# Kernel optimization log

Measured on AMD Instinct MI355X. Metric: run time of the kernel, lower is better.

Reference implementation:

```python
import jax, jax.numpy as jnp
import numpy as np

B, N, C = 4, 8192, 512
H, Dh, G, R = 8, 64, 64, 2  # heads, dim_head, slice_num, mlp_ratio
EPS_LN = 1e-5
EPS_NORM = 1e-5


def _ln(x, g, b):
    m = jnp.mean(x, axis=-1, keepdims=True)
    v = jnp.var(x, axis=-1, keepdims=True)
    return (x - m) * jax.lax.rsqrt(v + EPS_LN) * g + b


def setup_inputs() -> dict:
    key = jax.random.key(0)
    ks = jax.random.split(key, 16)
    r = lambda k, shp: jax.random.normal(k, shp, jnp.float32) * 0.02
    inner = H * Dh
    return {
        "fx": jax.random.normal(ks[0], (B, N, C), jnp.float32),
        "ln1_g": jnp.ones((C,), jnp.float32), "ln1_b": jnp.zeros((C,), jnp.float32),
        "Wx": r(ks[1], (C, inner)), "bx": jnp.zeros((inner,), jnp.float32),
        "Wfx": r(ks[2], (C, inner)), "bfx": jnp.zeros((inner,), jnp.float32),
        "Wslice": r(ks[3], (Dh, G)), "bslice": jnp.zeros((G,), jnp.float32),
        "temperature": jnp.full((1, H, 1, 1), 0.5, jnp.float32),
        "Wq": r(ks[4], (Dh, Dh)), "Wk": r(ks[5], (Dh, Dh)), "Wv": r(ks[6], (Dh, Dh)),
        "Wout": r(ks[7], (inner, C)), "bout": jnp.zeros((C,), jnp.float32),
        "tln_g": jnp.ones((Dh,), jnp.float32), "tln_b": jnp.zeros((Dh,), jnp.float32),
        "Wm1": r(ks[8], (Dh, R * Dh)), "bm1": jnp.zeros((R * Dh,), jnp.float32),
        "Wm2": r(ks[9], (R * Dh, Dh)), "bm2": jnp.zeros((Dh,), jnp.float32),
    }


def reference(fx, ln1_g, ln1_b, Wx, bx, Wfx, bfx, Wslice, bslice, temperature,
              Wq, Wk, Wv, Wout, bout, tln_g, tln_b, Wm1, bm1, Wm2, bm2):
    fx_norm = _ln(fx, ln1_g, ln1_b)                          # [B,N,C]
    # _forward_slice: project to per-head mid features
    x_mid = (fx_norm @ Wx + bx).reshape(B, N, H, Dh).transpose(0, 2, 1, 3)   # [B,H,N,Dh]
    fx_mid = (fx_norm @ Wfx + bfx).reshape(B, N, H, Dh).transpose(0, 2, 1, 3)
    # _project_token: soft slice assignment + weighted pooling into G tokens
    logits = jnp.einsum('bhnd,dg->bhng', x_mid, Wslice) + bslice
    slice_w = jax.nn.softmax(logits / temperature, axis=-1)  # [B,H,N,G]
    slice_norm = jnp.sum(slice_w, axis=2)                    # [B,H,G]
    slice_tok = jnp.einsum('bhnd,bhng->bhgd', fx_mid, slice_w) / (slice_norm[..., None] + EPS_NORM)
    # attention over the small token set (G tokens)
    q = slice_tok @ Wq
    k = slice_tok @ Wk
    v = slice_tok @ Wv
    scale = Dh ** -0.5
    attn = jax.nn.softmax(jnp.einsum('bhgd,bhpd->bhgp', q, k) * scale, axis=-1)
    out_tok = jnp.einsum('bhgp,bhpd->bhgd', attn, v) + slice_tok
    # token MLP with residual
    h = _ln(out_tok, tln_g, tln_b)
    h = jax.nn.gelu(h @ Wm1 + bm1, approximate=False) @ Wm2 + bm2
    tokens = h + out_tok                                     # [B,H,G,Dh]
    # _deslice: weighted scatter back to N points, merge heads, out projection
    out_x = jnp.einsum('bhgd,bhng->bhnd', tokens, slice_w)
    out_x = out_x.transpose(0, 2, 1, 3).reshape(B, N, H * Dh)
    out = out_x @ Wout + bout
    return out + fx_norm
```

## Files before the change

### kernel.cpp

```cpp
#include <hip/hip_runtime.h>
#include <math.h>

#define B_ 4
#define N_ 8192
#define C_ 512
#define H_ 8
#define M_ (B_ * N_)

typedef __attribute__((ext_vector_type(8))) short bf16x8;
typedef __attribute__((ext_vector_type(4))) float f32x4;
typedef __attribute__((ext_vector_type(8))) unsigned short u16x8;
typedef __attribute__((ext_vector_type(4))) unsigned short u16x4;

__device__ __forceinline__ float b2f(unsigned short u) {
  union { unsigned int i; float f; } v;
  v.i = ((unsigned int)u) << 16;
  return v.f;
}
__device__ __forceinline__ unsigned short f2b(float f) {
  union { float f; unsigned int i; } v;
  v.f = f;
  unsigned int r = v.i + 0x7fff + ((v.i >> 16) & 1);
  return (unsigned short)(r >> 16);
}
__device__ __forceinline__ void gl_lds16(const void* g, void* l) {
  __builtin_amdgcn_global_load_lds(
      (const __attribute__((address_space(1))) unsigned int*)g,
      (__attribute__((address_space(3))) unsigned int*)l, 16, 0, 0);
}

__global__ __launch_bounds__(256) void ln_bf16(
    const float* __restrict__ x, const float* __restrict__ gam,
    const float* __restrict__ bet, unsigned short* __restrict__ y) {
  int wave = threadIdx.x >> 6, lane = threadIdx.x & 63;
  int row = (blockIdx.x << 2) + wave;
  const float4* xr = (const float4*)(x + (size_t)row * C_);
  float4 v0 = xr[lane], v1 = xr[lane + 64];
  float s = v0.x + v0.y + v0.z + v0.w + v1.x + v1.y + v1.z + v1.w;
  float q = v0.x * v0.x + v0.y * v0.y + v0.z * v0.z + v0.w * v0.w +
            v1.x * v1.x + v1.y * v1.y + v1.z * v1.z + v1.w * v1.w;
#pragma unroll
  for (int off = 32; off; off >>= 1) {
    s += __shfl_xor(s, off);
    q += __shfl_xor(q, off);
  }
  float mean = s * (1.0f / C_);
  float var = q * (1.0f / C_) - mean * mean;
  float rstd = rsqrtf(var + 1e-5f);
  const float4* gr = (const float4*)gam;
  const float4* br = (const float4*)bet;
  float4 g0 = gr[lane], g1 = gr[lane + 64];
  float4 b0 = br[lane], b1 = br[lane + 64];
  u16x4 oa, ob;
  oa.x = f2b((v0.x - mean) * rstd * g0.x + b0.x);
  oa.y = f2b((v0.y - mean) * rstd * g0.y + b0.y);
  oa.z = f2b((v0.z - mean) * rstd * g0.z + b0.z);
  oa.w = f2b((v0.w - mean) * rstd * g0.w + b0.w);
  ob.x = f2b((v1.x - mean) * rstd * g1.x + b1.x);
  ob.y = f2b((v1.y - mean) * rstd * g1.y + b1.y);
  ob.z = f2b((v1.z - mean) * rstd * g1.z + b1.z);
  ob.w = f2b((v1.w - mean) * rstd * g1.w + b1.w);
  unsigned short* yr = y + (size_t)row * C_;
  *(u16x4*)(yr + (lane << 2)) = oa;
  *(u16x4*)(yr + 256 + (lane << 2)) = ob;
}

__global__ __launch_bounds__(256) void prep_all(
    const float* __restrict__ Wx, const float* __restrict__ Wfx,
    const float* __restrict__ Wout, const float* __restrict__ Wsl,
    const float* __restrict__ Wq, const float* __restrict__ Wk,
    const float* __restrict__ Wv, const float* __restrict__ Wm1,
    const float* __restrict__ Wm2, unsigned short* __restrict__ WtX,
    unsigned short* __restrict__ WtF, unsigned short* __restrict__ WtO,
    unsigned short* __restrict__ wsf, unsigned short* __restrict__ wfr) {
  __shared__ float tile[64][65];
  int blk = blockIdx.x, t = threadIdx.x;
  if (blk < 192) {
    int which = blk >> 6, sub = blk & 63;
    const float* W = (which == 0) ? Wx : (which == 1) ? Wfx : Wout;
    unsigned short* Wt = (which == 0) ? WtX : (which == 1) ? WtF : WtO;
    int r0 = (sub >> 3) << 6, c0 = (sub & 7) << 6;
    int lr = t >> 4, lc = (t & 15) << 2;
#pragma unroll
    for (int p = 0; p < 4; p++) {
      float4 v = *(const float4*)(W + (size_t)(r0 + lr + p * 16) * 512 + c0 + lc);
      tile[lr + p * 16][lc + 0] = v.x;
      tile[lr + p * 16][lc + 1] = v.y;
      tile[lr + p * 16][lc + 2] = v.z;
      tile[lr + p * 16][lc + 3] = v.w;
    }
    __syncthreads();
    int on = t >> 2, ok = (t & 3) << 4;
    unsigned short tmp[16];
#pragma unroll
    for (int j = 0; j < 16; j++) tmp[j] = f2b(tile[ok + j][on]);
    unsigned short* op = Wt + (size_t)(c0 + on) * 512 + r0 + ok;
#pragma unroll
    for (int j4 = 0; j4 < 4; j4++)
      *(u16x4*)(op + (j4 << 2)) = *(u16x4*)(tmp + (j4 << 2));
  } else {
#pragma unroll
    for (int i = 0; i < 2; i++) {
      int idx = t + i * 256;
      int f = idx >> 6, l = idx & 63;
      int gt = f >> 1, ks = f & 1;
      int g = (gt << 4) + (l & 15);
      int d0 = (ks << 5) + ((l >> 4) << 3);
      unsigned short v[8];
#pragma unroll
      for (int jj = 0; jj < 8; jj++) v[jj] = f2b(Wsl[(size_t)(d0 + jj) * 64 + g]);
      *(u16x4*)(wsf + idx * 8) = *(u16x4*)v;
      *(u16x4*)(wsf + idx * 8 + 4) = *(u16x4*)(v + 4);
    }
    for (int task = t; task < 56 * 64; task += 256) {
      int fid = task >> 6, l = task & 63;
      const float* W;
      int stride, ct, ks;
      if (fid < 24) {
        W = (fid < 8) ? Wq : (fid < 16) ? Wk : Wv;
        int e = fid & 7;
        ct = e >> 1;
        ks = e & 1;
        stride = 64;
      } else if (fid < 40) {
        W = Wm1;
        int e = fid - 24;
        ct = e >> 1;
        ks = e & 1;
        stride = 128;
      } else {
        W = Wm2;
        int e = fid - 40;
        ct = e >> 2;
        ks = e & 3;
        stride = 64;
      }
      int d0 = (ks << 5) + ((l >> 4) << 3);
      int c = (ct << 4) + (l & 15);
      unsigned short v[8];
#pragma unroll
      for (int j = 0; j < 8; j++) v[j] = f2b(W[(size_t)(d0 + j) * stride + c]);
      *(u16x4*)(wfr + task * 8) = *(u16x4*)v;
      *(u16x4*)(wfr + task * 8 + 4) = *(u16x4*)(v + 4);
    }
  }
}

template <int DEC, bool BIASROW, bool OUTBF, bool RES>
__global__ __launch_bounds__(256) void gemm_bf16(
    const unsigned short* __restrict__ A, const unsigned short* __restrict__ Bt,
    const float* __restrict__ bias, const unsigned short* __restrict__ resid,
    void* __restrict__ Cout, size_t ldC) {
  __shared__ unsigned short lds[16384];
  const int t = threadIdx.x;
  const int w = t >> 6, l = t & 63;
  int bid = blockIdx.x;
  int xcd = bid & 7, q = bid >> 3;
  int bm, bn;
  if (DEC == 0) {
    bm = ((xcd << 5) + (q >> 2)) << 7;
    bn = (q & 3) << 7;
  } else {
    bn = ((xcd << 5) + (q >> 2)) << 7;
    bm = (q & 3) << 7;
  }
  const int wm = (w >> 1) << 6, wn = (w & 1) << 6;
  f32x4 acc[4][4];
#pragma unroll
  for (int mt = 0; mt < 4; mt++)
#pragma unroll
    for (int nt = 0; nt < 4; nt++) acc[mt][nt] = (f32x4){0.f, 0.f, 0.f, 0.f};

  const int srow = t >> 3;
  const int scol = (((t & 7) ^ ((t >> 3) & 7)) << 3);
  const unsigned short* gA = A + (size_t)(bm + srow) * 512 + scol;
  const unsigned short* gB = Bt + (size_t)(bn + srow) * 512 + scol;
  const int fr = l & 15, qq = l >> 4;

  for (int k0 = 0; k0 < 512; k0 += 64) {
#pragma unroll
    for (int i = 0; i < 4; i++)
      gl_lds16(gA + (size_t)(i << 5) * 512 + k0, lds + (i << 11) + (w << 9));
#pragma unroll
    for (int i = 0; i < 4; i++)
      gl_lds16(gB + (size_t)(i << 5) * 512 + k0, lds + 8192 + (i << 11) + (w << 9));
    __syncthreads();
#pragma unroll
    for (int kk = 0; kk < 2; kk++) {
      bf16x8 af[4], bfr[4];
#pragma unroll
      for (int mt = 0; mt < 4; mt++) {
        int row = wm + mt * 16 + fr;
        af[mt] = *(const bf16x8*)&lds[row * 64 + ((((kk << 2) + qq) ^ (fr & 7)) << 3)];
      }
#pragma unroll
      for (int nt = 0; nt < 4; nt++) {
        int row = wn + nt * 16 + fr;
        bfr[nt] = *(const bf16x8*)&lds[8192 + row * 64 + ((((kk << 2) + qq) ^ (fr & 7)) << 3)];
      }
#pragma unroll
      for (int mt = 0; mt < 4; mt++)
#pragma unroll
        for (int nt = 0; nt < 4; nt++)
          acc[mt][nt] = __builtin_amdgcn_mfma_f32_16x16x32_bf16(
              af[mt], bfr[nt], acc[mt][nt], 0, 0, 0);
    }
    __syncthreads();
  }

  const int col0 = bn + wn + (l & 15);
  const int row0 = bm + wm + ((l >> 4) << 2);
#pragma unroll
  for (int mt = 0; mt < 4; mt++) {
#pragma unroll
    for (int j = 0; j < 4; j++) {
      int row = row0 + mt * 16 + j;
#pragma unroll
      for (int nt = 0; nt < 4; nt++) {
        int col = col0 + nt * 16;
        float v = acc[mt][nt][j] + (BIASROW ? bias[row] : bias[col]);
        if (RES) v += b2f(resid[(size_t)row * ldC + col]);
        if (OUTBF)
          ((unsigned short*)Cout)[(size_t)row * ldC + col] = f2b(v);
        else
          ((float*)Cout)[(size_t)row * ldC + col] = v;
      }
    }
  }
}

__global__ __launch_bounds__(256) void slice_mfma(
    unsigned short* __restrict__ xw, const unsigned short* __restrict__ wf,
    const float* __restrict__ bslice, const float* __restrict__ temp) {
  __shared__ unsigned short xs[4096];
  int t = threadIdx.x, w = t >> 6, l = t & 63;
  int blk = blockIdx.x;
  size_t base = (size_t)blk << 12;
  {
    int srow = t >> 2;
    const unsigned short* gp = xw + base + srow * 64 + ((t & 3) << 4);
    u16x8 a = *(const u16x8*)gp;
    u16x8 b = *(const u16x8*)(gp + 8);
    int sl0 = (t & 3) << 1, swz = srow & 7;
    *(u16x8*)&xs[srow * 64 + ((sl0 ^ swz) << 3)] = a;
    *(u16x8*)&xs[srow * 64 + (((sl0 + 1) ^ swz) << 3)] = b;
  }
  bf16x8 wsf[4][2];
#pragma unroll
  for (int gt = 0; gt < 4; gt++)
#pragma unroll
    for (int ks = 0; ks < 2; ks++)
      wsf[gt][ks] = *(const bf16x8*)(wf + (((gt << 1) + ks) * 64 + l) * 8);
  __syncthreads();

  int xr = (w << 4) + (l & 15);
  f32x4 acc[4];
#pragma unroll
  for (int gt = 0; gt < 4; gt++) acc[gt] = (f32x4){0.f, 0.f, 0.f, 0.f};
#pragma unroll
  for (int ks = 0; ks < 2; ks++) {
    int slot = (ks << 2) + (l >> 4);
    bf16x8 xf = *(const bf16x8*)&xs[xr * 64 + ((slot ^ (xr & 7)) << 3)];
#pragma unroll
    for (int gt = 0; gt < 4; gt++)
      acc[gt] = __builtin_amdgcn_mfma_f32_16x16x32_bf16(wsf[gt][ks], xf,
                                                        acc[gt], 0, 0, 0);
  }

  int gxr = (blk << 6) + xr;
  float invt = 1.0f / temp[gxr & 7];
  int qq = l >> 4;
  float lg[16];
  float mx = -1e30f;
#pragma unroll
  for (int gt = 0; gt < 4; gt++)
#pragma unroll
    for (int r = 0; r < 4; r++) {
      float v = (acc[gt][r] + bslice[(gt << 4) + (qq << 2) + r]) * invt;
      lg[(gt << 2) + r] = v;
      mx = fmaxf(mx, v);
    }
  mx = fmaxf(mx, __shfl_xor(mx, 16));
  mx = fmaxf(mx, __shfl_xor(mx, 32));
  float ssum = 0.f;
#pragma unroll
  for (int i = 0; i < 16; i++) {
    lg[i] = expf(lg[i] - mx);
    ssum += lg[i];
  }
  ssum += __shfl_xor(ssum, 16);
  ssum += __shfl_xor(ssum, 32);
  float inv = 1.0f / ssum;
  __syncthreads();
#pragma unroll
  for (int gt = 0; gt < 4; gt++) {
    int slot = (gt << 1) + (qq >> 1);
    int off = ((slot ^ (xr & 7)) << 3) + ((qq & 1) << 2);
    u16x4 pk;
    pk.x = f2b(lg[(gt << 2) + 0] * inv);
    pk.y = f2b(lg[(gt << 2) + 1] * inv);
    pk.z = f2b(lg[(gt << 2) + 2] * inv);
    pk.w = f2b(lg[(gt << 2) + 3] * inv);
    *(u16x4*)&xs[xr * 64 + off] = pk;
  }
  __syncthreads();
  {
    int rr = (w << 4) + (l >> 2);
    int sl = (l & 3) << 1, swz = rr & 7;
    u16x8 o0 = *(const u16x8*)&xs[rr * 64 + ((sl ^ swz) << 3)];
    u16x8 o1 = *(const u16x8*)&xs[rr * 64 + (((sl + 1) ^ swz) << 3)];
    unsigned short* op = xw + base + rr * 64 + ((l & 3) << 4);
    *(u16x8*)op = o0;
    *(u16x8*)(op + 8) = o1;
  }
}

__global__ __launch_bounds__(256) void pool_mfma(
    const unsigned short* __restrict__ sw, const unsigned short* __restrict__ fxT,
    float* __restrict__ tok_part, float* __restrict__ norm_part) {
  __shared__ unsigned short wT[4096];
  int bid = blockIdx.x;
  int bh = bid >> 4, c = bid & 15;
  int b = bh >> 3, h = bh & 7;
  int t = threadIdx.x, w = t >> 6, l = t & 63;
  int n0 = c << 9;
  const int fr15 = l & 15, fs = l >> 4;
  f32x4 acc[4];
#pragma unroll
  for (int gt = 0; gt < 4; gt++) acc[gt] = (f32x4){0.f, 0.f, 0.f, 0.f};
  float nacc[4] = {0.f, 0.f, 0.f, 0.f};

  const unsigned short* fxrow =
      fxT + (size_t)(h * 64 + w * 16 + fr15) * 32768 + b * N_ + n0 + (fs << 3);

  for (int nn = 0; nn < 512; nn += 64) {
    size_t srow = ((size_t)(b * N_ + n0 + nn + l) * 8 + h) << 6;
    u16x8 a0 = *(const u16x8*)(sw + srow + w * 16);
    u16x8 a1 = *(const u16x8*)(sw + srow + w * 16 + 8);
    __syncthreads();
#pragma unroll
    for (int j = 0; j < 16; j++) {
      int g = (w << 4) + j;
      unsigned short v = (j < 8) ? (unsigned short)a0[j] : (unsigned short)a1[j - 8];
      wT[(g << 6) + (((l >> 3) ^ (g & 7)) << 3) + (l & 7)] = v;
    }
    __syncthreads();
#pragma unroll
    for (int kk = 0; kk < 2; kk++) {
      bf16x8 bfrag = *(const bf16x8*)(fxrow + nn + (kk << 5));
#pragma unroll
      for (int gt = 0; gt < 4; gt++) {
        int g = (gt << 4) + fr15;
        int slot = (kk << 2) + fs;
        bf16x8 af = *(const bf16x8*)&wT[(g << 6) + ((slot ^ (g & 7)) << 3)];
        acc[gt] = __builtin_amdgcn_mfma_f32_16x16x32_bf16(af, bfrag, acc[gt], 0, 0, 0);
        if (w == 0) {
#pragma unroll
          for (int j = 0; j < 8; j++) nacc[gt] += b2f((unsigned short)af[j]);
        }
      }
    }
  }
  float* op = tok_part + ((size_t)bid << 12);
#pragma unroll
  for (int gt = 0; gt < 4; gt++)
#pragma unroll
    for (int rr = 0; rr < 4; rr++)
      op[((gt << 4) + (fs << 2) + rr) * 64 + (w << 4) + fr15] = acc[gt][rr];
  if (w == 0) {
#pragma unroll
    for (int gt = 0; gt < 4; gt++) {
      float s = nacc[gt];
      s += __shfl_xor(s, 16);
      s += __shfl_xor(s, 32);
      if (l < 16) norm_part[(bid << 6) + (gt << 4) + l] = s;
    }
  }
}

__global__ __launch_bounds__(256) void tok_reduce(
    const float* __restrict__ tok_part, const float* __restrict__ norm_part,
    float* __restrict__ stG) {
  int blk = blockIdx.x;
  int bh = blk >> 2, qq = blk & 3;
  int t = threadIdx.x;
  int e = (qq << 10) + (t << 2);
  int g = e >> 6;
  float s = 0.f;
  const float* np = norm_part + ((size_t)bh << 10);
#pragma unroll
  for (int c = 0; c < 16; c++) s += np[(c << 6) + g];
  float4 acc = make_float4(0.f, 0.f, 0.f, 0.f);
  const float* tp = tok_part + ((size_t)bh << 16) + e;
#pragma unroll
  for (int c = 0; c < 16; c++) {
    float4 v = *(const float4*)(tp + (c << 12));
    acc.x += v.x;
    acc.y += v.y;
    acc.z += v.z;
    acc.w += v.w;
  }
  float inv = 1.0f / (s + 1e-5f);
  acc.x *= inv;
  acc.y *= inv;
  acc.z *= inv;
  acc.w *= inv;
  *(float4*)(stG + ((size_t)bh << 12) + e) = acc;
}

__device__ __forceinline__ float gelu_exact(float x) {
  return 0.5f * x * (1.0f + erff(x * 0.70710678118654752f));
}

__global__ __launch_bounds__(256) void token_mfma(
    const float* __restrict__ stG, const unsigned short* __restrict__ wfr,
    const float* __restrict__ tg, const float* __restrict__ tb,
    const float* __restrict__ bm1, const float* __restrict__ bm2,
    unsigned short* __restrict__ wtokf) {
  __shared__ __align__(16) char smem[54272];
  unsigned short* stb = (unsigned short*)smem;
  float* st32 = (float*)(smem + 9216);
  unsigned short* hmld = (unsigned short*)(smem + 9216);
  unsigned short* qld = (unsigned short*)(smem + 26624);
  unsigned short* kld = (unsigned short*)(smem + 35840);
  unsigned short* vtl = (unsigned short*)(smem + 45056);

  int bh = blockIdx.x, t = threadIdx.x, w = t >> 6, l = t & 63;
  const int fr = l & 15, fq = l >> 4;

  {
    int r = t >> 2, c0 = (t & 3) << 4;
    const float* gp = stG + ((size_t)bh << 12) + r * 64 + c0;
    float4 a = *(const float4*)gp;
    float4 b = *(const float4*)(gp + 4);
    float4 c = *(const float4*)(gp + 8);
    float4 d = *(const float4*)(gp + 12);
    *(float4*)&st32[r * 68 + c0] = a;
    *(float4*)&st32[r * 68 + c0 + 4] = b;
    *(float4*)&st32[r * 68 + c0 + 8] = c;
    *(float4*)&st32[r * 68 + c0 + 12] = d;
    unsigned short tv[16];
    tv[0] = f2b(a.x); tv[1] = f2b(a.y); tv[2] = f2b(a.z); tv[3] = f2b(a.w);
    tv[4] = f2b(b.x); tv[5] = f2b(b.y); tv[6] = f2b(b.z); tv[7] = f2b(b.w);
    tv[8] = f2b(c.x); tv[9] = f2b(c.y); tv[10] = f2b(c.z); tv[11] = f2b(c.w);
    tv[12] = f2b(d.x); tv[13] = f2b(d.y); tv[14] = f2b(d.z); tv[15] = f2b(d.w);
    *(u16x8*)&stb[r * 72 + c0] = *(u16x8*)tv;
    *(u16x8*)&stb[r * 72 + c0 + 8] = *(u16x8*)(tv + 8);
  }
  __syncthreads();

  const int orow = (w << 4) + (fq << 2);

  {
    bf16x8 af[2];
#pragma unroll
    for (int ks = 0; ks < 2; ks++)
      af[ks] = *(const bf16x8*)&stb[((w << 4) + fr) * 72 + (ks << 5) + (fq << 3)];
    f32x4 aq[4], ak[4], av[4];
#pragma unroll
    for (int ct = 0; ct < 4; ct++) {
      aq[ct] = (f32x4){0.f, 0.f, 0.f, 0.f};
      ak[ct] = (f32x4){0.f, 0.f, 0.f, 0.f};
      av[ct] = (f32x4){0.f, 0.f, 0.f, 0.f};
    }
#pragma unroll
    for (int ct = 0; ct < 4; ct++)
#pragma unroll
      for (int ks = 0; ks < 2; ks++) {
        bf16x8 bq = *(const bf16x8*)&wfr[(((ct << 1) + ks) * 64 + l) * 8];
        aq[ct] = __builtin_amdgcn_mfma_f32_16x16x32_bf16(af[ks], bq, aq[ct], 0, 0, 0);
      }
#pragma unroll
    for (int ct = 0; ct < 4; ct++)
#pragma unroll
      for (int ks = 0; ks < 2; ks++) {
        bf16x8 bk = *(const bf16x8*)&wfr[((8 + (ct << 1) + ks) * 64 + l) * 8];
        ak[ct] = __builtin_amdgcn_mfma_f32_16x16x32_bf16(af[ks], bk, ak[ct], 0, 0, 0);
      }
#pragma unroll
    for (int ct = 0; ct < 4; ct++)
#pragma unroll
      for (int ks = 0; ks < 2; ks++) {
        bf16x8 bv = *(const bf16x8*)&wfr[((16 + (ct << 1) + ks) * 64 + l) * 8];
        av[ct] = __builtin_amdgcn_mfma_f32_16x16x32_bf16(af[ks], bv, av[ct], 0, 0, 0);
      }
#pragma unroll
    for (int ct = 0; ct < 4; ct++) {
#pragma unroll
      for (int rr = 0; rr < 4; rr++) {
        qld[(orow + rr) * 72 + (ct << 4) + fr] = f2b(aq[ct][rr]);
        kld[(orow + rr) * 72 + (ct << 4) + fr] = f2b(ak[ct][rr]);
      }
      u16x4 vp;
      vp.x = f2b(av[ct][0]);
      vp.y = f2b(av[ct][1]);
      vp.z = f2b(av[ct][2]);
      vp.w = f2b(av[ct][3]);
      *(u16x4*)&vtl[((ct << 4) + fr) * 72 + orow] = vp;
    }
  }
  __syncthreads();

  {
    bf16x8 aq[2];
#pragma unroll
    for (int ks = 0; ks < 2; ks++)
      aq[ks] = *(const bf16x8*)&qld[((w << 4) + fr) * 72 + (ks << 5) + (fq << 3)];
    f32x4 accs[4];
#pragma unroll
    for (int nt = 0; nt < 4; nt++) accs[nt] = (f32x4){0.f, 0.f, 0.f, 0.f};
#pragma unroll
    for (int nt = 0; nt < 4; nt++)
#pragma unroll
      for (int ks = 0; ks < 2; ks++) {
        bf16x8 bk = *(const bf16x8*)&kld[((nt << 4) + fr) * 72 + (ks << 5) + (fq << 3)];
        accs[nt] = __builtin_amdgcn_mfma_f32_16x16x32_bf16(aq[ks], bk, accs[nt], 0, 0, 0);
      }
#pragma unroll
    for (int rr = 0; rr < 4; rr++) {
      float v0 = accs[0][rr] * 0.125f, v1 = accs[1][rr] * 0.125f;
      float v2 = accs[2][rr] * 0.125f, v3 = accs[3][rr] * 0.125f;
      float mx = fmaxf(fmaxf(v0, v1), fmaxf(v2, v3));
      mx = fmaxf(mx, __shfl_xor(mx, 1));
      mx = fmaxf(mx, __shfl_xor(mx, 2));
      mx = fmaxf(mx, __shfl_xor(mx, 4));
      mx = fmaxf(mx, __shfl_xor(mx, 8));
      float e0 = expf(v0 - mx), e1 = expf(v1 - mx);
      float e2 = expf(v2 - mx), e3 = expf(v3 - mx);
      float ss = e0 + e1 + e2 + e3;
      ss += __shfl_xor(ss, 1);
      ss += __shfl_xor(ss, 2);
      ss += __shfl_xor(ss, 4);
      ss += __shfl_xor(ss, 8);
      float inv = 1.0f / ss;
      stb[(orow + rr) * 72 + 0 * 16 + fr] = f2b(e0 * inv);
      stb[(orow + rr) * 72 + 1 * 16 + fr] = f2b(e1 * inv);
      stb[(orow + rr) * 72 + 2 * 16 + fr] = f2b(e2 * inv);
      stb[(orow + rr) * 72 + 3 * 16 + fr] = f2b(e3 * inv);
    }
  }
  __syncthreads();

  float o16[4][4];
  {
    bf16x8 ap[2];
#pragma unroll
    for (int ks = 0; ks < 2; ks++)
      ap[ks] = *(const bf16x8*)&stb[((w << 4) + fr) * 72 + (ks << 5) + (fq << 3)];
    f32x4 acco[4];
#pragma unroll
    for (int ct = 0; ct < 4; ct++) acco[ct] = (f32x4){0.f, 0.f, 0.f, 0.f};
#pragma unroll
    for (int ct = 0; ct < 4; ct++)
#pragma unroll
      for (int ks = 0; ks < 2; ks++) {
        bf16x8 bv = *(const bf16x8*)&vtl[((ct << 4) + fr) * 72 + (ks << 5) + (fq << 3)];
        acco[ct] = __builtin_amdgcn_mfma_f32_16x16x32_bf16(ap[ks], bv, acco[ct], 0, 0, 0);
      }
    float tgv[4], tbv[4];
#pragma unroll
    for (int ct = 0; ct < 4; ct++) {
      tgv[ct] = tg[(ct << 4) + fr];
      tbv[ct] = tb[(ct << 4) + fr];
    }
#pragma unroll
    for (int ct = 0; ct < 4; ct++)
#pragma unroll
      for (int rr = 0; rr < 4; rr++)
        o16[ct][rr] = acco[ct][rr] + st32[(orow + rr) * 68 + (ct << 4) + fr];
#pragma unroll
    for (int rr = 0; rr < 4; rr++) {
      float sm = o16[0][rr] + o16[1][rr] + o16[2][rr] + o16[3][rr];
      float sq = o16[0][rr] * o16[0][rr] + o16[1][rr] * o16[1][rr] +
                 o16[2][rr] * o16[2][rr] + o16[3][rr] * o16[3][rr];
      sm += __shfl_xor(sm, 1);
      sm += __shfl_xor(sm, 2);
      sm += __shfl_xor(sm, 4);
      sm += __shfl_xor(sm, 8);
      sq += __shfl_xor(sq, 1);
      sq += __shfl_xor(sq, 2);
      sq += __shfl_xor(sq, 4);
      sq += __shfl_xor(sq, 8);
      float mean = sm * (1.0f / 64.0f);
      float var = sq * (1.0f / 64.0f) - mean * mean;
      float rstd = rsqrtf(var + 1e-5f);
#pragma unroll
      for (int ct = 0; ct < 4; ct++) {
        float hv = (o16[ct][rr] - mean) * rstd * tgv[ct] + tbv[ct];
        qld[(orow + rr) * 72 + (ct << 4) + fr] = f2b(hv);
      }
    }
  }
  __syncthreads();

  {
    bf16x8 ah[2];
#pragma unroll
    for (int ks = 0; ks < 2; ks++)
      ah[ks] = *(const bf16x8*)&qld[((w << 4) + fr) * 72 + (ks << 5) + (fq << 3)];
    f32x4 accm[8];
#pragma unroll
    for (int et = 0; et < 8; et++) accm[et] = (f32x4){0.f, 0.f, 0.f, 0.f};
#pragma unroll
    for (int et = 0; et < 8; et++)
#pragma unroll
      for (int ks = 0; ks < 2; ks++) {
        bf16x8 bm = *(const bf16x8*)&wfr[((24 + (et << 1) + ks) * 64 + l) * 8];
        accm[et] = __builtin_amdgcn_mfma_f32_16x16x32_bf16(ah[ks], bm, accm[et], 0, 0, 0);
      }
#pragma unroll
    for (int et = 0; et < 8; et++) {
      float bv = bm1[(et << 4) + fr];
#pragma unroll
      for (int rr = 0; rr < 4; rr++) {
        float x = accm[et][rr] + bv;
        hmld[(orow + rr) * 136 + (et << 4) + fr] = f2b(gelu_exact(x));
      }
    }
  }
  __syncthreads();

  {
    bf16x8 ahm[4];
#pragma unroll
    for (int ks = 0; ks < 4; ks++)
      ahm[ks] = *(const bf16x8*)&hmld[((w << 4) + fr) * 136 + (ks << 5) + (fq << 3)];
    f32x4 acc2[4];
#pragma unroll
    for (int ct = 0; ct < 4; ct++) acc2[ct] = (f32x4){0.f, 0.f, 0.f, 0.f};
#pragma unroll
    for (int ct = 0; ct < 4; ct++)
#pragma unroll
      for (int ks = 0; ks < 4; ks++) {
        bf16x8 bw = *(const bf16x8*)&wfr[((40 + (ct << 2) + ks) * 64 + l) * 8];
        acc2[ct] = __builtin_amdgcn_mfma_f32_16x16x32_bf16(ahm[ks], bw, acc2[ct], 0, 0, 0);
      }
#pragma unroll
    for (int ct = 0; ct < 4; ct++) {
      float bv = bm2[(ct << 4) + fr];
#pragma unroll
      for (int rr = 0; rr < 4; rr++)
        stb[(orow + rr) * 72 + (ct << 4) + fr] =
            f2b(acc2[ct][rr] + bv + o16[ct][rr]);
    }
  }
  __syncthreads();
  {
#pragma unroll
    for (int e = 0; e < 2; e++) {
      int fid = (w << 1) + e;
      int d = (w << 4) + (l & 15);
      int g0 = (e << 5) + ((l >> 4) << 3);
      unsigned short v[8];
#pragma unroll
      for (int j = 0; j < 8; j++) v[j] = stb[(g0 + j) * 72 + d];
      unsigned short* op = wtokf + (((size_t)bh << 3) + fid) * 512 + (l << 3);
      *(u16x4*)op = *(u16x4*)v;
      *(u16x4*)(op + 4) = *(u16x4*)(v + 4);
    }
  }
}

__global__ __launch_bounds__(256) void deslice_mfma(
    const unsigned short* __restrict__ wtokf, const unsigned short* __restrict__ sw,
    unsigned short* __restrict__ outx) {
  int bid = blockIdx.x;
  int bh = bid >> 4, c = bid & 15;
  int b = bh >> 3, h = bh & 7;
  int t = threadIdx.x, w = t >> 6, l = t & 63;
  const int fr = l & 15, fq = l >> 4;

  bf16x8 ta[4][2];
  const unsigned short* fp = wtokf + ((size_t)bh << 12);
#pragma unroll
  for (int mt = 0; mt < 4; mt++)
#pragma unroll
    for (int ks = 0; ks < 2; ks++)
      ta[mt][ks] = *(const bf16x8*)(fp + (((mt << 1) + ks) << 9) + (l << 3));

  int n0 = (c << 9) + (w << 7);
#pragma unroll 2
  for (int ntile = 0; ntile < 8; ntile++) {
    int nb = n0 + (ntile << 4);
    size_t rowb = ((size_t)(b * N_ + nb + fr) * 8 + h) << 6;
    bf16x8 b0 = *(const bf16x8*)(sw + rowb + (fq << 3));
    bf16x8 b1 = *(const bf16x8*)(sw + rowb + 32 + (fq << 3));
    f32x4 acc[4];
#pragma unroll
    for (int mt = 0; mt < 4; mt++) acc[mt] = (f32x4){0.f, 0.f, 0.f, 0.f};
#pragma unroll
    for (int mt = 0; mt < 4; mt++) {
      acc[mt] = __builtin_amdgcn_mfma_f32_16x16x32_bf16(ta[mt][0], b0, acc[mt], 0, 0, 0);
      acc[mt] = __builtin_amdgcn_mfma_f32_16x16x32_bf16(ta[mt][1], b1, acc[mt], 0, 0, 0);
    }
    unsigned short* op = outx + rowb + (fq << 2);
#pragma unroll
    for (int mt = 0; mt < 4; mt++) {
      u16x4 pk;
      pk.x = f2b(acc[mt][0]);
      pk.y = f2b(acc[mt][1]);
      pk.z = f2b(acc[mt][2]);
      pk.w = f2b(acc[mt][3]);
      *(u16x4*)(op + (mt << 4)) = pk;
    }
  }
}

extern "C" void kernel_launch(void* const* d_in, const int* in_sizes, int n_in,
                              void* d_out, int out_size, void* d_ws,
                              size_t ws_size, hipStream_t stream) {
  const float* fx = (const float*)d_in[0];
  const float* ln1g = (const float*)d_in[1];
  const float* ln1b = (const float*)d_in[2];
  const float* Wx = (const float*)d_in[3];
  const float* bx = (const float*)d_in[4];
  const float* Wfx = (const float*)d_in[5];
  const float* bfx = (const float*)d_in[6];
  const float* Wsl = (const float*)d_in[7];
  const float* bsl = (const float*)d_in[8];
  const float* temp = (const float*)d_in[9];
  const float* Wq = (const float*)d_in[10];
  const float* Wk = (const float*)d_in[11];
  const float* Wv = (const float*)d_in[12];
  const float* Wout = (const float*)d_in[13];
  const float* bout = (const float*)d_in[14];
  const float* tlng = (const float*)d_in[15];
  const float* tlnb = (const float*)d_in[16];
  const float* Wm1 = (const float*)d_in[17];
  const float* bm1 = (const float*)d_in[18];
  const float* Wm2 = (const float*)d_in[19];
  const float* bm2 = (const float*)d_in[20];
  float* out = (float*)d_out;

  char* p = (char*)d_ws;
  const size_t MC2 = (size_t)M_ * 512 * 2;
  unsigned short* fxn = (unsigned short*)p;  p += MC2;
  unsigned short* buf1 = (unsigned short*)p; p += MC2;
  unsigned short* bufT = (unsigned short*)p; p += MC2;
  unsigned short* WtX = (unsigned short*)p;  p += 512 * 512 * 2;
  unsigned short* WtF = (unsigned short*)p;  p += 512 * 512 * 2;
  unsigned short* WtO = (unsigned short*)p;  p += 512 * 512 * 2;
  unsigned short* wsf = (unsigned short*)p;  p += 8192;
  unsigned short* wfr = (unsigned short*)p;  p += 56 * 512 * 2;
  unsigned short* wtokf = (unsigned short*)p; p += (size_t)32 * 8 * 512 * 2;
  float* tok_part = (float*)p;  p += (size_t)512 * 4096 * 4;
  float* norm_part = (float*)p; p += (size_t)512 * 64 * 4;
  float* stG = (float*)p;       p += (size_t)32 * 4096 * 4;

  ln_bf16<<<M_ / 4, 256, 0, stream>>>(fx, ln1g, ln1b, fxn);
  prep_all<<<193, 256, 0, stream>>>(Wx, Wfx, Wout, Wsl, Wq, Wk, Wv, Wm1, Wm2,
                                    WtX, WtF, WtO, wsf, wfr);
  gemm_bf16<0, false, true, false><<<1024, 256, 0, stream>>>(fxn, WtX, bx, nullptr, buf1, 512);
  gemm_bf16<1, true, true, false><<<1024, 256, 0, stream>>>(WtF, fxn, bfx, nullptr, bufT, 32768);
  slice_mfma<<<4096, 256, 0, stream>>>(buf1, wsf, bsl, temp);
  pool_mfma<<<512, 256, 0, stream>>>(buf1, bufT, tok_part, norm_part);
  tok_reduce<<<128, 256, 0, stream>>>(tok_part, norm_part, stG);
  token_mfma<<<32, 256, 0, stream>>>(stG, wfr, tlng, tlnb, bm1, bm2, wtokf);
  deslice_mfma<<<512, 256, 0, stream>>>(wtokf, buf1, bufT);
  gemm_bf16<0, false, false, true><<<1024, 256, 0, stream>>>(bufT, WtO, bout, fxn, out, 512);
}
```

Measured before the change: 172.5 us.

## Fuse slice softmax into pool and deslice; fold token reduce into token kernel

Removes the standalone slice_mfma kernel. The slice-logit MFMA and softmax are now recomputed inside both pool_mfma and deslice_mfma from x_mid, so the slice weights are never written to and read back from global memory. The tok_reduce kernel is also folded into token_mfma, which now sums the partial tokens and norms itself. This cuts two launches and one full read-write pass over the 32 MB buffer, at the cost of computing the softmax twice and extra LDS traffic inside deslice.

```diff
diff --git a/kernel.cpp b/kernel.cpp
--- a/kernel.cpp
+++ b/kernel.cpp
@@ -229,95 +229,11 @@
   }
 }
 
-__global__ __launch_bounds__(256) void slice_mfma(
-    unsigned short* __restrict__ xw, const unsigned short* __restrict__ wf,
-    const float* __restrict__ bslice, const float* __restrict__ temp) {
-  __shared__ unsigned short xs[4096];
-  int t = threadIdx.x, w = t >> 6, l = t & 63;
-  int blk = blockIdx.x;
-  size_t base = (size_t)blk << 12;
-  {
-    int srow = t >> 2;
-    const unsigned short* gp = xw + base + srow * 64 + ((t & 3) << 4);
-    u16x8 a = *(const u16x8*)gp;
-    u16x8 b = *(const u16x8*)(gp + 8);
-    int sl0 = (t & 3) << 1, swz = srow & 7;
-    *(u16x8*)&xs[srow * 64 + ((sl0 ^ swz) << 3)] = a;
-    *(u16x8*)&xs[srow * 64 + (((sl0 + 1) ^ swz) << 3)] = b;
-  }
-  bf16x8 wsf[4][2];
-#pragma unroll
-  for (int gt = 0; gt < 4; gt++)
-#pragma unroll
-    for (int ks = 0; ks < 2; ks++)
-      wsf[gt][ks] = *(const bf16x8*)(wf + (((gt << 1) + ks) * 64 + l) * 8);
-  __syncthreads();
-
-  int xr = (w << 4) + (l & 15);
-  f32x4 acc[4];
-#pragma unroll
-  for (int gt = 0; gt < 4; gt++) acc[gt] = (f32x4){0.f, 0.f, 0.f, 0.f};
-#pragma unroll
-  for (int ks = 0; ks < 2; ks++) {
-    int slot = (ks << 2) + (l >> 4);
-    bf16x8 xf = *(const bf16x8*)&xs[xr * 64 + ((slot ^ (xr & 7)) << 3)];
-#pragma unroll
-    for (int gt = 0; gt < 4; gt++)
-      acc[gt] = __builtin_amdgcn_mfma_f32_16x16x32_bf16(wsf[gt][ks], xf,
-                                                        acc[gt], 0, 0, 0);
-  }
-
-  int gxr = (blk << 6) + xr;
-  float invt = 1.0f / temp[gxr & 7];
-  int qq = l >> 4;
-  float lg[16];
-  float mx = -1e30f;
-#pragma unroll
-  for (int gt = 0; gt < 4; gt++)
-#pragma unroll
-    for (int r = 0; r < 4; r++) {
-      float v = (acc[gt][r] + bslice[(gt << 4) + (qq << 2) + r]) * invt;
-      lg[(gt << 2) + r] = v;
-      mx = fmaxf(mx, v);
-    }
-  mx = fmaxf(mx, __shfl_xor(mx, 16));
-  mx = fmaxf(mx, __shfl_xor(mx, 32));
-  float ssum = 0.f;
-#pragma unroll
-  for (int i = 0; i < 16; i++) {
-    lg[i] = expf(lg[i] - mx);
-    ssum += lg[i];
-  }
-  ssum += __shfl_xor(ssum, 16);
-  ssum += __shfl_xor(ssum, 32);
-  float inv = 1.0f / ssum;
-  __syncthreads();
-#pragma unroll
-  for (int gt = 0; gt < 4; gt++) {
-    int slot = (gt << 1) + (qq >> 1);
-    int off = ((slot ^ (xr & 7)) << 3) + ((qq & 1) << 2);
-    u16x4 pk;
-    pk.x = f2b(lg[(gt << 2) + 0] * inv);
-    pk.y = f2b(lg[(gt << 2) + 1] * inv);
-    pk.z = f2b(lg[(gt << 2) + 2] * inv);
-    pk.w = f2b(lg[(gt << 2) + 3] * inv);
-    *(u16x4*)&xs[xr * 64 + off] = pk;
-  }
-  __syncthreads();
-  {
-    int rr = (w << 4) + (l >> 2);
-    int sl = (l & 3) << 1, swz = rr & 7;
-    u16x8 o0 = *(const u16x8*)&xs[rr * 64 + ((sl ^ swz) << 3)];
-    u16x8 o1 = *(const u16x8*)&xs[rr * 64 + (((sl + 1) ^ swz) << 3)];
-    unsigned short* op = xw + base + rr * 64 + ((l & 3) << 4);
-    *(u16x8*)op = o0;
-    *(u16x8*)(op + 8) = o1;
-  }
-}
-
 __global__ __launch_bounds__(256) void pool_mfma(
-    const unsigned short* __restrict__ sw, const unsigned short* __restrict__ fxT,
-    float* __restrict__ tok_part, float* __restrict__ norm_part) {
+    const unsigned short* __restrict__ xmid, const unsigned short* __restrict__ fxT,
+    const unsigned short* __restrict__ wf, const float* __restrict__ bslice,
+    const float* __restrict__ temp, float* __restrict__ tok_part,
+    float* __restrict__ norm_part) {
   __shared__ unsigned short wT[4096];
   int bid = blockIdx.x;
   int bh = bid >> 4, c = bid & 15;
@@ -325,6 +241,21 @@
   int t = threadIdx.x, w = t >> 6, l = t & 63;
   int n0 = c << 9;
   const int fr15 = l & 15, fs = l >> 4;
+
+  bf16x8 wsf[4][2];
+#pragma unroll
+  for (int gt = 0; gt < 4; gt++)
+#pragma unroll
+    for (int ks = 0; ks < 2; ks++)
+      wsf[gt][ks] = *(const bf16x8*)(wf + (((gt << 1) + ks) * 64 + l) * 8);
+  float invt = 1.0f / temp[h];
+  float bsl16[16];
+#pragma unroll
+  for (int gt = 0; gt < 4; gt++)
+#pragma unroll
+    for (int r = 0; r < 4; r++)
+      bsl16[(gt << 2) + r] = bslice[(gt << 4) + (fs << 2) + r];
+
   f32x4 acc[4];
 #pragma unroll
   for (int gt = 0; gt < 4; gt++) acc[gt] = (f32x4){0.f, 0.f, 0.f, 0.f};
@@ -332,18 +263,49 @@
 
   const unsigned short* fxrow =
       fxT + (size_t)(h * 64 + w * 16 + fr15) * 32768 + b * N_ + n0 + (fs << 3);
+  const int ncol = (w << 4) + fr15;
 
   for (int nn = 0; nn < 512; nn += 64) {
-    size_t srow = ((size_t)(b * N_ + n0 + nn + l) * 8 + h) << 6;
-    u16x8 a0 = *(const u16x8*)(sw + srow + w * 16);
-    u16x8 a1 = *(const u16x8*)(sw + srow + w * 16 + 8);
+    size_t xrow = ((size_t)(b * N_ + n0 + nn + ncol) * 8 + h) << 6;
+    bf16x8 xf0 = *(const bf16x8*)(xmid + xrow + (fs << 3));
+    bf16x8 xf1 = *(const bf16x8*)(xmid + xrow + 32 + (fs << 3));
+    f32x4 lg4[4];
+#pragma unroll
+    for (int gt = 0; gt < 4; gt++) {
+      lg4[gt] = (f32x4){0.f, 0.f, 0.f, 0.f};
+      lg4[gt] = __builtin_amdgcn_mfma_f32_16x16x32_bf16(wsf[gt][0], xf0, lg4[gt], 0, 0, 0);
+      lg4[gt] = __builtin_amdgcn_mfma_f32_16x16x32_bf16(wsf[gt][1], xf1, lg4[gt], 0, 0, 0);
+    }
+    float p[16];
+    float mx = -1e30f;
+#pragma unroll
+    for (int gt = 0; gt < 4; gt++)
+#pragma unroll
+      for (int r = 0; r < 4; r++) {
+        float v = (lg4[gt][r] + bsl16[(gt << 2) + r]) * invt;
+        p[(gt << 2) + r] = v;
+        mx = fmaxf(mx, v);
+      }
+    mx = fmaxf(mx, __shfl_xor(mx, 16));
+    mx = fmaxf(mx, __shfl_xor(mx, 32));
+    float ssum = 0.f;
+#pragma unroll
+    for (int i = 0; i < 16; i++) {
+      p[i] = expf(p[i] - mx);
+      ssum += p[i];
+    }
+    ssum += __shfl_xor(ssum, 16);
+    ssum += __shfl_xor(ssum, 32);
+    float inv = 1.0f / ssum;
     __syncthreads();
 #pragma unroll
-    for (int j = 0; j < 16; j++) {
-      int g = (w << 4) + j;
-      unsigned short v = (j < 8) ? (unsigned short)a0[j] : (unsigned short)a1[j - 8];
-      wT[(g << 6) + (((l >> 3) ^ (g & 7)) << 3) + (l & 7)] = v;
-    }
+    for (int gt = 0; gt < 4; gt++)
+#pragma unroll
+      for (int r = 0; r < 4; r++) {
+        int g = (gt << 4) + (fs << 2) + r;
+        wT[(g << 6) + ((((ncol >> 3)) ^ (g & 7)) << 3) + (ncol & 7)] =
+            f2b(p[(gt << 2) + r] * inv);
+      }
     __syncthreads();
 #pragma unroll
     for (int kk = 0; kk < 2; kk++) {
@@ -378,46 +340,17 @@
   }
 }
 
-__global__ __launch_bounds__(256) void tok_reduce(
-    const float* __restrict__ tok_part, const float* __restrict__ norm_part,
-    float* __restrict__ stG) {
-  int blk = blockIdx.x;
-  int bh = blk >> 2, qq = blk & 3;
-  int t = threadIdx.x;
-  int e = (qq << 10) + (t << 2);
-  int g = e >> 6;
-  float s = 0.f;
-  const float* np = norm_part + ((size_t)bh << 10);
-#pragma unroll
-  for (int c = 0; c < 16; c++) s += np[(c << 6) + g];
-  float4 acc = make_float4(0.f, 0.f, 0.f, 0.f);
-  const float* tp = tok_part + ((size_t)bh << 16) + e;
-#pragma unroll
-  for (int c = 0; c < 16; c++) {
-    float4 v = *(const float4*)(tp + (c << 12));
-    acc.x += v.x;
-    acc.y += v.y;
-    acc.z += v.z;
-    acc.w += v.w;
-  }
-  float inv = 1.0f / (s + 1e-5f);
-  acc.x *= inv;
-  acc.y *= inv;
-  acc.z *= inv;
-  acc.w *= inv;
-  *(float4*)(stG + ((size_t)bh << 12) + e) = acc;
-}
-
 __device__ __forceinline__ float gelu_exact(float x) {
   return 0.5f * x * (1.0f + erff(x * 0.70710678118654752f));
 }
 
 __global__ __launch_bounds__(256) void token_mfma(
-    const float* __restrict__ stG, const unsigned short* __restrict__ wfr,
-    const float* __restrict__ tg, const float* __restrict__ tb,
-    const float* __restrict__ bm1, const float* __restrict__ bm2,
-    unsigned short* __restrict__ wtokf) {
+    const float* __restrict__ tok_part, const float* __restrict__ norm_part,
+    const unsigned short* __restrict__ wfr, const float* __restrict__ tg,
+    const float* __restrict__ tb, const float* __restrict__ bm1,
+    const float* __restrict__ bm2, unsigned short* __restrict__ wtokf) {
   __shared__ __align__(16) char smem[54272];
+  __shared__ float red[64];
   unsigned short* stb = (unsigned short*)smem;
   float* st32 = (float*)(smem + 9216);
   unsigned short* hmld = (unsigned short*)(smem + 9216);
@@ -428,22 +361,39 @@
   int bh = blockIdx.x, t = threadIdx.x, w = t >> 6, l = t & 63;
   const int fr = l & 15, fq = l >> 4;
 
+  if (t < 64) {
+    float s = 0.f;
+    const float* np = norm_part + ((size_t)bh << 10);
+#pragma unroll
+    for (int cc = 0; cc < 16; cc++) s += np[(cc << 6) + t];
+    red[t] = s;
+  }
   {
+    float a16[16];
+#pragma unroll
+    for (int j = 0; j < 16; j++) a16[j] = 0.f;
+    const float* tp = tok_part + ((size_t)bh << 16) + (t << 4);
+    for (int cc = 0; cc < 16; cc++) {
+      const float* pp = tp + (cc << 12);
+#pragma unroll
+      for (int j4 = 0; j4 < 4; j4++) {
+        float4 v = *(const float4*)(pp + (j4 << 2));
+        a16[j4 * 4 + 0] += v.x;
+        a16[j4 * 4 + 1] += v.y;
+        a16[j4 * 4 + 2] += v.z;
+        a16[j4 * 4 + 3] += v.w;
+      }
+    }
+    __syncthreads();
+    float rn = 1.0f / (red[t >> 2] + 1e-5f);
     int r = t >> 2, c0 = (t & 3) << 4;
-    const float* gp = stG + ((size_t)bh << 12) + r * 64 + c0;
-    float4 a = *(const float4*)gp;
-    float4 b = *(const float4*)(gp + 4);
-    float4 c = *(const float4*)(gp + 8);
-    float4 d = *(const float4*)(gp + 12);
-    *(float4*)&st32[r * 68 + c0] = a;
-    *(float4*)&st32[r * 68 + c0 + 4] = b;
-    *(float4*)&st32[r * 68 + c0 + 8] = c;
-    *(float4*)&st32[r * 68 + c0 + 12] = d;
     unsigned short tv[16];
-    tv[0] = f2b(a.x); tv[1] = f2b(a.y); tv[2] = f2b(a.z); tv[3] = f2b(a.w);
-    tv[4] = f2b(b.x); tv[5] = f2b(b.y); tv[6] = f2b(b.z); tv[7] = f2b(b.w);
-    tv[8] = f2b(c.x); tv[9] = f2b(c.y); tv[10] = f2b(c.z); tv[11] = f2b(c.w);
-    tv[12] = f2b(d.x); tv[13] = f2b(d.y); tv[14] = f2b(d.z); tv[15] = f2b(d.w);
+#pragma unroll
+    for (int j = 0; j < 16; j++) {
+      float v = a16[j] * rn;
+      st32[r * 68 + c0 + j] = v;
+      tv[j] = f2b(v);
+    }
     *(u16x8*)&stb[r * 72 + c0] = *(u16x8*)tv;
     *(u16x8*)&stb[r * 72 + c0 + 8] = *(u16x8*)(tv + 8);
   }
@@ -662,13 +612,16 @@
 }
 
 __global__ __launch_bounds__(256) void deslice_mfma(
-    const unsigned short* __restrict__ wtokf, const unsigned short* __restrict__ sw,
-    unsigned short* __restrict__ outx) {
+    const unsigned short* __restrict__ wtokf, const unsigned short* __restrict__ xmid,
+    const unsigned short* __restrict__ wf, const float* __restrict__ bslice,
+    const float* __restrict__ temp, unsigned short* __restrict__ outx) {
+  __shared__ unsigned short pex[4][1024];
   int bid = blockIdx.x;
   int bh = bid >> 4, c = bid & 15;
   int b = bh >> 3, h = bh & 7;
   int t = threadIdx.x, w = t >> 6, l = t & 63;
   const int fr = l & 15, fq = l >> 4;
+  unsigned short* pw = pex[w];
 
   bf16x8 ta[4][2];
   const unsigned short* fp = wtokf + ((size_t)bh << 12);
@@ -677,14 +630,64 @@
 #pragma unroll
     for (int ks = 0; ks < 2; ks++)
       ta[mt][ks] = *(const bf16x8*)(fp + (((mt << 1) + ks) << 9) + (l << 3));
+  bf16x8 wsf[4][2];
+#pragma unroll
+  for (int gt = 0; gt < 4; gt++)
+#pragma unroll
+    for (int ks = 0; ks < 2; ks++)
+      wsf[gt][ks] = *(const bf16x8*)(wf + (((gt << 1) + ks) * 64 + l) * 8);
+  float invt = 1.0f / temp[h];
+  float bsl16[16];
+#pragma unroll
+  for (int gt = 0; gt < 4; gt++)
+#pragma unroll
+    for (int r = 0; r < 4; r++)
+      bsl16[(gt << 2) + r] = bslice[(gt << 4) + (fq << 2) + r];
 
   int n0 = (c << 9) + (w << 7);
-#pragma unroll 2
   for (int ntile = 0; ntile < 8; ntile++) {
     int nb = n0 + (ntile << 4);
     size_t rowb = ((size_t)(b * N_ + nb + fr) * 8 + h) << 6;
-    bf16x8 b0 = *(const bf16x8*)(sw + rowb + (fq << 3));
-    bf16x8 b1 = *(const bf16x8*)(sw + rowb + 32 + (fq << 3));
+    bf16x8 xf0 = *(const bf16x8*)(xmid + rowb + (fq << 3));
+    bf16x8 xf1 = *(const bf16x8*)(xmid + rowb + 32 + (fq << 3));
+    f32x4 lg4[4];
+#pragma unroll
+    for (int gt = 0; gt < 4; gt++) {
+      lg4[gt] = (f32x4){0.f, 0.f, 0.f, 0.f};
+      lg4[gt] = __builtin_amdgcn_mfma_f32_16x16x32_bf16(wsf[gt][0], xf0, lg4[gt], 0, 0, 0);
+      lg4[gt] = __builtin_amdgcn_mfma_f32_16x16x32_bf16(wsf[gt][1], xf1, lg4[gt], 0, 0, 0);
+    }
+    float p[16];
+    float mx = -1e30f;
+#pragma unroll
+    for (int gt = 0; gt < 4; gt++)
+#pragma unroll
+      for (int r = 0; r < 4; r++) {
+        float v = (lg4[gt][r] + bsl16[(gt << 2) + r]) * invt;
+        p[(gt << 2) + r] = v;
+        mx = fmaxf(mx, v);
+      }
+    mx = fmaxf(mx, __shfl_xor(mx, 16));
+    mx = fmaxf(mx, __shfl_xor(mx, 32));
+    float ssum = 0.f;
+#pragma unroll
+    for (int i = 0; i < 16; i++) {
+      p[i] = expf(p[i] - mx);
+      ssum += p[i];
+    }
+    ssum += __shfl_xor(ssum, 16);
+    ssum += __shfl_xor(ssum, 32);
+    float inv = 1.0f / ssum;
+#pragma unroll
+    for (int gt = 0; gt < 4; gt++)
+#pragma unroll
+      for (int r = 0; r < 4; r++) {
+        int g = (gt << 4) + (fq << 2) + r;
+        pw[(fr << 6) + (((g >> 3) ^ (fr & 7)) << 3) + (g & 7)] =
+            f2b(p[(gt << 2) + r] * inv);
+      }
+    bf16x8 b0 = *(const bf16x8*)&pw[(fr << 6) + ((fq ^ (fr & 7)) << 3)];
+    bf16x8 b1 = *(const bf16x8*)&pw[(fr << 6) + (((4 + fq) ^ (fr & 7)) << 3)];
     f32x4 acc[4];
 #pragma unroll
     for (int mt = 0; mt < 4; mt++) acc[mt] = (f32x4){0.f, 0.f, 0.f, 0.f};
@@ -745,17 +748,14 @@
   unsigned short* wtokf = (unsigned short*)p; p += (size_t)32 * 8 * 512 * 2;
   float* tok_part = (float*)p;  p += (size_t)512 * 4096 * 4;
   float* norm_part = (float*)p; p += (size_t)512 * 64 * 4;
-  float* stG = (float*)p;       p += (size_t)32 * 4096 * 4;
 
   ln_bf16<<<M_ / 4, 256, 0, stream>>>(fx, ln1g, ln1b, fxn);
   prep_all<<<193, 256, 0, stream>>>(Wx, Wfx, Wout, Wsl, Wq, Wk, Wv, Wm1, Wm2,
                                     WtX, WtF, WtO, wsf, wfr);
   gemm_bf16<0, false, true, false><<<1024, 256, 0, stream>>>(fxn, WtX, bx, nullptr, buf1, 512);
   gemm_bf16<1, true, true, false><<<1024, 256, 0, stream>>>(WtF, fxn, bfx, nullptr, bufT, 32768);
-  slice_mfma<<<4096, 256, 0, stream>>>(buf1, wsf, bsl, temp);
-  pool_mfma<<<512, 256, 0, stream>>>(buf1, bufT, tok_part, norm_part);
-  tok_reduce<<<128, 256, 0, stream>>>(tok_part, norm_part, stG);
-  token_mfma<<<32, 256, 0, stream>>>(stG, wfr, tlng, tlnb, bm1, bm2, wtokf);
-  deslice_mfma<<<512, 256, 0, stream>>>(wtokf, buf1, bufT);
+  pool_mfma<<<512, 256, 0, stream>>>(buf1, bufT, wsf, bsl, temp, tok_part, norm_part);
+  token_mfma<<<32, 256, 0, stream>>>(tok_part, norm_part, wfr, tlng, tlnb, bm1, bm2, wtokf);
+  deslice_mfma<<<512, 256, 0, stream>>>(wtokf, buf1, wsf, bsl, temp, bufT);
   gemm_bf16<0, false, false, true><<<1024, 256, 0, stream>>>(bufT, WtO, bout, fxn, out, 512);
 }
```

Measured after the change: 171.8 us. No clear change (-0.4%).
